# Performance work log

Hardware: AMD Instinct MI355X
Metric: run time of the kernel (lower is better)

## Reference

```python
import jax, jax.numpy as jnp
import numpy as np

B, T, C, H, E, MIN_E = 4, 2048, 1024, 128, 16, 2
IS_CAUSAL = False


def setup_inputs() -> dict:
    key = jax.random.key(0)
    ks = jax.random.split(key, 6)
    lim_qkv = float(np.sqrt(6.0 / (C + H)))
    inp = {
        "hidden_states": jax.random.normal(ks[0], (B, T, C), jnp.float32),
        "sim_matrix": jax.random.normal(ks[1], (C, E), jnp.float32),
        "gates": jnp.zeros((E,), jnp.float32),
        "q_proj": jax.random.uniform(ks[2], (E, C, H), jnp.float32, -lim_qkv, lim_qkv),
        "k_proj": jax.random.uniform(ks[3], (E, C, H), jnp.float32, -lim_qkv, lim_qkv),
        "v_proj": jax.random.uniform(ks[4], (E, C, H), jnp.float32, -lim_qkv, lim_qkv),
        "o_proj": jax.random.uniform(ks[5], (E, H, C), jnp.float32, -lim_qkv, lim_qkv),
    }
    return inp


def _forward(hidden_states, sim_matrix, gates, q_proj, k_proj, v_proj, o_proj):
    b, t, c = hidden_states.shape
    n = b * t
    x = hidden_states.reshape(n, c)

    # ---- gating (faithful to _gating_logic) ----
    xn = x / jnp.maximum(jnp.linalg.norm(x, axis=-1, keepdims=True), 1e-12)
    sn = sim_matrix / jnp.maximum(jnp.linalg.norm(sim_matrix, axis=0, keepdims=True), 1e-12)
    logits = xn @ sn - jax.nn.sigmoid(gates)          # [n, E]
    gated = jax.nn.relu(logits)
    # STE: forward = (gated > 0), backward = identity
    hard = (gated > 0).astype(gated.dtype)
    mask = gated + jax.lax.stop_gradient(hard - gated)
    inactive = (jnp.sum(hard, axis=1) == 0)
    # fallback: top-MIN_E logits for tokens with no active expert
    _, fb_idx = jax.lax.top_k(logits, MIN_E)
    fb = jnp.zeros((n, logits.shape[1]), gated.dtype).at[
        jnp.arange(n)[:, None], fb_idx].set(1.0)
    put = jax.lax.stop_gradient(inactive[:, None].astype(gated.dtype) * fb)
    mask = mask * (1.0 - put) + put                   # index_put semantics
    masked = jnp.where(mask > 0, gated, -jnp.inf)
    w = jax.nn.softmax(masked, axis=-1)               # routing weights [n, E]

    # ---- MoE dispatch/combine (dense-equivalent: w is exactly 0 where mask==0) ----
    def moe_proj(p):  # p: [E, C, H] -> [n, H]
        y = jnp.einsum('nc,ech->neh', x, p)
        return jnp.einsum('ne,neh->nh', w, y)

    q = moe_proj(q_proj).reshape(b, t, -1)
    k = moe_proj(k_proj).reshape(b, t, -1)
    v = moe_proj(v_proj).reshape(b, t, -1)

    # single-head SDPA, default scale 1/sqrt(head_dim)
    h = q.shape[-1]
    scores = jnp.einsum('bth,bsh->bts', q, k) / jnp.sqrt(jnp.asarray(h, q.dtype))
    if IS_CAUSAL and t > 1:
        causal = jnp.tril(jnp.ones((t, t), bool))
        scores = jnp.where(causal[None], scores, -jnp.inf)
    attn = jax.nn.softmax(scores, axis=-1)
    o = jnp.einsum('bts,bsh->bth', attn, v).reshape(n, h)

    # output MoE combine
    z = jnp.einsum('ne,nh->enh', w, o)                # [E, n, H]
    out = jnp.einsum('enh,ehc->nc', z, o_proj)
    return out.reshape(b, t, c)


def reference(hidden_states, sim_matrix, gates, q_proj, k_proj, v_proj, o_proj):
    return _forward(hidden_states, sim_matrix, gates, q_proj, k_proj, v_proj, o_proj)
```

## Files before the change

### kernel.cpp

```cpp
#include <hip/hip_runtime.h>
#include <hip/hip_bf16.h>
#include <math.h>

#define NBATCH 4
#define NT     2048
#define NC     1024
#define NH     128
#define NE     16
#define NTOK   (NBATCH * NT)
#define CAP    18432
#define NT2_MAX 152

typedef __bf16 bf16x8 __attribute__((ext_vector_type(8)));
typedef __bf16 bf16x4 __attribute__((ext_vector_type(4)));
typedef float  f32x4  __attribute__((ext_vector_type(4)));

__device__ __forceinline__ __bf16 f2bf(float f) { return (__bf16)f; }

#define BARRIER() __builtin_amdgcn_s_barrier()
#define SFENCE()  __builtin_amdgcn_sched_barrier(0)
#define VMWAIT(n) asm volatile("s_waitcnt vmcnt(" #n ")" ::: "memory")
#define LGKMWAIT0() asm volatile("s_waitcnt lgkmcnt(0)" ::: "memory")

__device__ __forceinline__ void gl_lds16(const void* g, void* l) {
  __builtin_amdgcn_global_load_lds((const __attribute__((address_space(1))) void*)g,
                                   (__attribute__((address_space(3))) void*)l, 16, 0, 0);
}

__device__ __forceinline__ const __bf16* swz_src(const __bf16* row0, size_t stride,
                                                 int tid, int i) {
  int lin = (tid + 256 * i) * 16;
  int r = lin >> 7, cb = lin & 127;
  return row0 + (size_t)r * stride + ((cb ^ ((r & 7) << 4)) >> 1);
}

__device__ __forceinline__ bool locate_tile(const int* __restrict__ counts, int ti,
                                            int& e_out, int& s0_out, int& seg_end_out) {
  int off = 0, nt = 0, e = -1, s0 = 0, seg_end = 0;
#pragma unroll
  for (int ee = 0; ee < NE; ee++) {
    int c = counts[ee];
    int tiles = (c + 127) >> 7;
    if (e < 0 && ti < nt + tiles) {
      e = ee;
      s0 = off + (ti - nt) * 128;
      seg_end = off + c;
    }
    nt += tiles;
    off += c;
  }
  if (e < 0 || s0 >= CAP) return false;
  if (seg_end > CAP) seg_end = CAP;
  e_out = e; s0_out = s0; seg_end_out = seg_end;
  return true;
}

__global__ void k_transpose_all(const float* __restrict__ qp, const float* __restrict__ kp,
                                const float* __restrict__ vp, const float* __restrict__ op,
                                __bf16* __restrict__ pqt, __bf16* __restrict__ pkt,
                                __bf16* __restrict__ pvt, __bf16* __restrict__ pot,
                                const float* __restrict__ sim, const float* __restrict__ gates,
                                double* __restrict__ snorm, double* __restrict__ sig,
                                int* __restrict__ ctrl) {
  __shared__ float tile[32][33];
  __shared__ double red[16][17];
  int z = blockIdx.y;
  int tid = threadIdx.x;
  if (z == 64) {
    if (blockIdx.x != 0) return;
    if (tid < 128) ctrl[tid] = 0;
    int e = tid & 15, chunk = tid >> 4;
    double a = 0.0;
#pragma unroll 4
    for (int j = 0; j < 64; j++) {
      double v = (double)sim[(chunk * 64 + j) * NE + e];
      a += v * v;
    }
    red[chunk][e] = a;
    __syncthreads();
    if (tid < 16) {
      double s = 0.0;
      for (int k = 0; k < 16; k++) s += red[k][tid];
      snorm[tid] = fmax(sqrt(s), 1e-12);
      sig[tid] = 1.0 / (1.0 + exp(-(double)gates[tid]));
    }
    return;
  }
  const float* in;
  __bf16* out;
  int R, Cd, g, r0, c0;
  if (z < 48) {
    int which = z >> 4; g = z & 15; R = 1024; Cd = 128;
    in = which == 0 ? qp : (which == 1 ? kp : vp);
    out = which == 0 ? pqt : (which == 1 ? pkt : pvt);
    r0 = (blockIdx.x >> 2) * 32; c0 = (blockIdx.x & 3) * 32;
  } else {
    g = z - 48; R = 128; Cd = 1024;
    in = op; out = pot;
    r0 = (blockIdx.x & 3) * 32; c0 = (blockIdx.x >> 2) * 32;
  }
  int tx = tid & 31, ty0 = tid >> 5;
  const float* src = in + (size_t)g * R * Cd;
  __bf16* dst = out + (size_t)g * R * Cd;
#pragma unroll
  for (int ty = ty0; ty < 32; ty += 8)
    tile[ty][tx] = src[(size_t)(r0 + ty) * Cd + (c0 + tx)];
  __syncthreads();
#pragma unroll
  for (int ty = ty0; ty < 32; ty += 8)
    dst[(size_t)(c0 + ty) * R + (r0 + tx)] = f2bf(tile[tx][ty]);
}

__global__ __launch_bounds__(256, 2) void k_gating3(const float* __restrict__ x,
                                                    const float* __restrict__ sim,
                                                    const double* __restrict__ snorm,
                                                    const double* __restrict__ sig,
                                                    float* __restrict__ w_all,
                                                    int* __restrict__ counts,
                                                    __bf16* __restrict__ xbf) {
  __shared__ union {
    struct {
      float xs_[16][66];
      float ss_[16][66];
    } s;
    double red[8][32][2][17];
  } u;
  __shared__ float w_lds[16][16];
  __shared__ int cnt_lds[16];
  int tid = threadIdx.x;
  if (tid < 16) cnt_lds[tid] = 0;
  int cg = tid & 31, tkg = tid >> 5;
  int tok0 = blockIdx.x * 16;

  double acc[2][17];
#pragma unroll
  for (int t = 0; t < 2; t++)
#pragma unroll
    for (int i = 0; i < 17; i++) acc[t][i] = 0.0;

  int xr0 = tid >> 4, xc4 = (tid & 15) * 4;
  int sr = tid >> 2, se4 = (tid & 3) * 4;

  float4 xa, sv;
  auto ldchunk = [&](int c0) {
    xa = *(const float4*)(x + (size_t)(tok0 + xr0) * NC + c0 + xc4);
    sv = *(const float4*)(sim + (size_t)(c0 + sr) * NE + se4);
  };
  auto stchunk = [&]() {
    *(float4*)&u.s.xs_[xr0][xc4] = xa;
    u.s.ss_[se4 + 0][sr] = sv.x;
    u.s.ss_[se4 + 1][sr] = sv.y;
    u.s.ss_[se4 + 2][sr] = sv.z;
    u.s.ss_[se4 + 3][sr] = sv.w;
  };
  auto stxbf = [&](int c0) {
    bf16x4 a;
    a[0]=f2bf(xa.x); a[1]=f2bf(xa.y); a[2]=f2bf(xa.z); a[3]=f2bf(xa.w);
    *(bf16x4*)(xbf + (size_t)(tok0 + xr0) * NC + c0 + xc4) = a;
  };

  ldchunk(0);
  for (int ch = 0; ch < 16; ch++) {
    stchunk();
    stxbf(ch * 64);
    __syncthreads();
    if (ch < 15) ldchunk((ch + 1) * 64);
    double xd[2][2];
#pragma unroll
    for (int t = 0; t < 2; t++) {
      float2 xv = *(const float2*)&u.s.xs_[tkg * 2 + t][cg * 2];
      xd[t][0] = (double)xv.x;
      xd[t][1] = (double)xv.y;
      acc[t][16] += xd[t][0] * xd[t][0] + xd[t][1] * xd[t][1];
    }
#pragma unroll
    for (int e = 0; e < 16; e++) {
      float2 sv2 = *(const float2*)&u.s.ss_[e][cg * 2];
      double s0 = (double)sv2.x, s1 = (double)sv2.y;
#pragma unroll
      for (int t = 0; t < 2; t++)
        acc[t][e] += xd[t][0] * s0 + xd[t][1] * s1;
    }
    __syncthreads();
  }

#pragma unroll
  for (int t = 0; t < 2; t++)
#pragma unroll
    for (int i = 0; i < 17; i++)
      u.red[tkg][cg][t][i] = acc[t][i];
  __syncthreads();

  if (tid < 16) {
    double dots[17];
    for (int i = 0; i < 17; i++) {
      double s = 0.0;
      for (int c = 0; c < 32; c++) s += u.red[tid >> 1][c][tid & 1][i];
      dots[i] = s;
    }
    double xn = fmax(sqrt(dots[16]), 1e-12);
    double logits[NE];
    unsigned act = 0;
    int cnt = 0;
    for (int ee = 0; ee < NE; ee++) {
      logits[ee] = dots[ee] / (xn * snorm[ee]) - sig[ee];
      if (logits[ee] > 0.0) { act |= 1u << ee; cnt++; }
    }
    if (cnt == 0) {
      int i1 = 0; double b1 = logits[0];
      for (int ee = 1; ee < NE; ee++) if (logits[ee] > b1) { b1 = logits[ee]; i1 = ee; }
      int i2 = -1; double b2 = -1e300;
      for (int ee = 0; ee < NE; ee++) if (ee != i1 && logits[ee] > b2) { b2 = logits[ee]; i2 = ee; }
      act = (1u << i1) | (1u << i2);
    }
    double m = -1e300;
    for (int ee = 0; ee < NE; ee++) if ((act >> ee) & 1) m = fmax(m, fmax(logits[ee], 0.0));
    double s = 0.0, wvv[NE];
    for (int ee = 0; ee < NE; ee++) {
      if ((act >> ee) & 1) { wvv[ee] = exp(fmax(logits[ee], 0.0) - m); s += wvv[ee]; }
      else wvv[ee] = 0.0;
    }
    for (int ee = 0; ee < NE; ee++) {
      if ((act >> ee) & 1) {
        w_lds[tid][ee] = (float)(wvv[ee] / s);
        atomicAdd(&cnt_lds[ee], 1);
      } else w_lds[tid][ee] = 0.0f;
    }
  }
  __syncthreads();
  w_all[(size_t)(tok0 + (tid >> 4)) * NE + (tid & 15)] = w_lds[tid >> 4][tid & 15];
  if (tid < 16 && cnt_lds[tid] > 0) atomicAdd(&counts[tid], cnt_lds[tid]);
}

__global__ void k_assign(const float* __restrict__ w_all, const int* __restrict__ counts,
                         int* __restrict__ cursors, int* __restrict__ slot_token,
                         float* __restrict__ slot_w, int* __restrict__ tok_slots,
                         int* __restrict__ tok_cnt) {
  int n = blockIdx.x * 256 + threadIdx.x;
  int lane = threadIdx.x & 63;
  int j = 0;
  int off = 0;
#pragma unroll
  for (int e = 0; e < NE; e++) {
    float w = w_all[(size_t)n * NE + e];
    bool a = w > 0.0f;
    unsigned long long mask = __ballot(a);
    if (mask) {
      int leader = (int)__ffsll((long long)mask) - 1;
      int base = 0;
      if (lane == leader) base = atomicAdd(&cursors[e], (int)__popcll(mask));
      base = __shfl(base, leader);
      if (a) {
        int pos = base + (int)__popcll(mask & ((1ULL << lane) - 1ULL));
        int s = off + pos;
        slot_token[s] = n;
        slot_w[s] = w;
        tok_slots[n * 16 + j] = s;
        j++;
      }
    }
    off += counts[e];
  }
  tok_cnt[n] = j;
}

__device__ __forceinline__ void mfma_block(const __bf16* As, const __bf16* Bs,
                                           int lane, int wrow, f32x4 acc[8]) {
  const char* Ab = (const char*)As;
  const char* Bb = (const char*)Bs;
  int arow = wrow + (lane & 15);
  int rb = lane & 15;
#pragma unroll
  for (int ks = 0; ks < 2; ks++) {
    int kb = ks * 64 + (lane >> 4) * 16;
    bf16x8 af = *(const bf16x8*)(Ab + arow * 128 + (kb ^ ((arow & 7) << 4)));
#pragma unroll
    for (int nt = 0; nt < 8; nt++) {
      int brow = nt * 16 + rb;
      bf16x8 bv = *(const bf16x8*)(Bb + brow * 128 + (kb ^ ((brow & 7) << 4)));
      acc[nt] = __builtin_amdgcn_mfma_f32_16x16x32_bf16(af, bv, acc[nt], 0, 0, 0);
    }
  }
}

__device__ __forceinline__ void mfma_block128(const __bf16* As, const __bf16* Bs,
                                              int lane, int wrow2, f32x4 acc[2][8]) {
  const char* Ab = (const char*)As;
  const char* Bb = (const char*)Bs;
  int rb = lane & 15;
#pragma unroll
  for (int ks = 0; ks < 2; ks++) {
    int kb = ks * 64 + (lane >> 4) * 16;
    int ar = wrow2 + rb;
    int sw = kb ^ ((ar & 7) << 4);
    bf16x8 af0 = *(const bf16x8*)(Ab + ar * 128 + sw);
    bf16x8 af1 = *(const bf16x8*)(Ab + (ar + 16) * 128 + sw);
#pragma unroll
    for (int nt = 0; nt < 8; nt++) {
      int brow = nt * 16 + rb;
      bf16x8 bv = *(const bf16x8*)(Bb + brow * 128 + (kb ^ ((brow & 7) << 4)));
      acc[0][nt] = __builtin_amdgcn_mfma_f32_16x16x32_bf16(af0, bv, acc[0][nt], 0, 0, 0);
      acc[1][nt] = __builtin_amdgcn_mfma_f32_16x16x32_bf16(af1, bv, acc[1][nt], 0, 0, 0);
    }
  }
}

__device__ __forceinline__ void mfma_regA(bf16x8 af0, bf16x8 af1, const __bf16* Bs,
                                          int lane, f32x4 acc[8]) {
  const char* Bb = (const char*)Bs;
  int rb = lane & 15;
#pragma unroll
  for (int ks = 0; ks < 2; ks++) {
    int kb = ks * 64 + (lane >> 4) * 16;
    bf16x8 af = ks ? af1 : af0;
#pragma unroll
    for (int nt = 0; nt < 8; nt++) {
      int brow = nt * 16 + rb;
      bf16x8 bv = *(const bf16x8*)(Bb + brow * 128 + (kb ^ ((brow & 7) << 4)));
      acc[nt] = __builtin_amdgcn_mfma_f32_16x16x32_bf16(af, bv, acc[nt], 0, 0, 0);
    }
  }
}

__global__ __launch_bounds__(256) void k_moe_qkv2(
    const __bf16* __restrict__ xbf, const int* __restrict__ slot_token,
    const __bf16* __restrict__ pq, const __bf16* __restrict__ pk, const __bf16* __restrict__ pv,
    const int* __restrict__ counts,
    __bf16* __restrict__ yq, __bf16* __restrict__ yk, __bf16* __restrict__ yv) {
  int id = blockIdx.x;
  int w = (id & 7) * (3 * NT2_MAX / 8) + (id >> 3);
  int ti = w / 3, p = w % 3;
  int e, s0, seg_end;
  if (!locate_tile(counts, ti, e, s0, seg_end)) return;
  const __bf16* Bt;
  __bf16* Yd;
  if (p == 0)      { Bt = pq; Yd = yq; }
  else if (p == 1) { Bt = pk; Yd = yk; }
  else             { Bt = pv; Yd = yv; }
  Bt += (size_t)e * NH * NC;

  __shared__ __bf16 As[2][128 * 64];
  __shared__ __bf16 Bs[2][128 * 64];
  int tid = threadIdx.x, lane = tid & 63, wid = tid >> 6, wrow2 = wid * 32;
  const __bf16* asrc[4];
  const __bf16* bsrc[4];
#pragma unroll
  for (int i = 0; i < 4; i++) {
    int lin = (tid + 256 * i) * 16;
    int r = lin >> 7, cb = lin & 127;
    int tok = slot_token[s0 + r] & (NTOK - 1);
    asrc[i] = xbf + (size_t)tok * NC + ((cb ^ ((r & 7) << 4)) >> 1);
  }
#pragma unroll
  for (int i = 0; i < 4; i++) bsrc[i] = swz_src(Bt, NC, tid, i);
  auto stage = [&](int buf, int k0) {
#pragma unroll
    for (int i = 0; i < 4; i++)
      gl_lds16(asrc[i] + k0, (char*)As[buf] + tid * 16 + i * 4096);
#pragma unroll
    for (int i = 0; i < 4; i++)
      gl_lds16(bsrc[i] + k0, (char*)Bs[buf] + tid * 16 + i * 4096);
  };

  f32x4 acc[2][8];
#pragma unroll
  for (int rf = 0; rf < 2; rf++)
#pragma unroll
    for (int i = 0; i < 8; i++) { f32x4 z = {0.f, 0.f, 0.f, 0.f}; acc[rf][i] = z; }

  stage(0, 0);
  stage(1, 64);
  VMWAIT(8); BARRIER(); SFENCE();
  int cur = 0;
  for (int t = 0; t <= 13; t++) {
    __builtin_amdgcn_s_setprio(1);
    mfma_block128(As[cur], Bs[cur], lane, wrow2, acc);
    __builtin_amdgcn_s_setprio(0);
    SFENCE();
    BARRIER();
    stage(cur, (t + 2) * 64);
    VMWAIT(8); BARRIER(); SFENCE();
    cur ^= 1;
  }
  __builtin_amdgcn_s_setprio(1);
  mfma_block128(As[cur], Bs[cur], lane, wrow2, acc);
  __builtin_amdgcn_s_setprio(0);
  SFENCE();
  VMWAIT(0); BARRIER(); SFENCE();
  __builtin_amdgcn_s_setprio(1);
  mfma_block128(As[cur ^ 1], Bs[cur ^ 1], lane, wrow2, acc);
  __builtin_amdgcn_s_setprio(0);

  int col = lane & 15, quad = lane >> 4;
#pragma unroll
  for (int rf = 0; rf < 2; rf++)
#pragma unroll
    for (int r = 0; r < 4; r++) {
      int s = s0 + wrow2 + rf * 16 + quad * 4 + r;
      if (s < seg_end) {
#pragma unroll
        for (int nt = 0; nt < 8; nt++)
          Yd[(size_t)s * NH + nt * 16 + col] = f2bf(acc[rf][nt][r]);
      }
    }
}

__global__ __launch_bounds__(256) void k_combine_qkv(
    const __bf16* __restrict__ yq, const __bf16* __restrict__ yk, const __bf16* __restrict__ yv,
    const int* __restrict__ tok_slots, const int* __restrict__ tok_cnt,
    const float* __restrict__ slot_w,
    __bf16* __restrict__ qb, __bf16* __restrict__ kb, __bf16* __restrict__ vt) {
  __shared__ __bf16 vtile[128][34];
  int tid = threadIdx.x;
  int tok0 = blockIdx.x * 32;
  int tt = tok0 + (tid >> 3);
  int h0 = (tid & 7) * 16;
  const __bf16* Y = blockIdx.y == 0 ? yq : (blockIdx.y == 1 ? yk : yv);
  int cnt = tok_cnt[tt];
  float acc[16];
#pragma unroll
  for (int i = 0; i < 16; i++) acc[i] = 0.f;
  for (int j = 0; j < cnt; j++) {
    int s = tok_slots[tt * 16 + j];
    if (s < CAP) {
      float w = slot_w[s];
      bf16x8 v0 = *(const bf16x8*)(Y + (size_t)s * NH + h0);
      bf16x8 v1 = *(const bf16x8*)(Y + (size_t)s * NH + h0 + 8);
#pragma unroll
      for (int i = 0; i < 8; i++) { acc[i] += w * (float)v0[i]; acc[8 + i] += w * (float)v1[i]; }
    }
  }
  if (blockIdx.y == 2) {
#pragma unroll
    for (int i = 0; i < 16; i++) vtile[h0 + i][tid >> 3] = f2bf(acc[i]);
    __syncthreads();
    int h = tid >> 1, tp = (tid & 1) * 16;
    int b = tok0 >> 11, trow = tok0 & 2047;
    __bf16* dst = vt + ((size_t)b * NH + h) * NT + trow + tp;
    bf16x8 o0, o1;
#pragma unroll
    for (int i = 0; i < 8; i++) { o0[i] = vtile[h][tp + i]; o1[i] = vtile[h][tp + 8 + i]; }
    *(bf16x8*)dst = o0;
    *(bf16x8*)(dst + 8) = o1;
  } else {
    float sc = blockIdx.y == 0 ? 0.12751744458115337f : 1.0f;
    __bf16* D = blockIdx.y == 0 ? qb : kb;
    bf16x8 o0, o1;
#pragma unroll
    for (int i = 0; i < 8; i++) { o0[i] = f2bf(acc[i] * sc); o1[i] = f2bf(acc[8 + i] * sc); }
    __bf16* d = D + (size_t)tt * NH + h0;
    *(bf16x8*)d = o0;
    *(bf16x8*)(d + 8) = o1;
  }
}

__global__ __launch_bounds__(256) void k_flash(const __bf16* __restrict__ q,
                                               const __bf16* __restrict__ k,
                                               const __bf16* __restrict__ vt,
                                               float* __restrict__ opart,
                                               float2* __restrict__ ml) {
  int id = blockIdx.x;
  int w = (id & 7) * 64 + (id >> 3);
  int b = w >> 7;
  int rem = w & 127;
  int spl = rem >> 5;
  int t0 = (rem & 31) * 64;
  const __bf16* qb = q + (size_t)b * NT * NH;
  const __bf16* kb = k + (size_t)b * NT * NH;
  const __bf16* vtb = vt + (size_t)b * NH * NT;

  __shared__ __bf16 Ks[2][128 * 64];
  __shared__ __bf16 Vs[2][128 * 64];
  __shared__ __bf16 Ps[2][64 * 64];
  int tid = threadIdx.x, lane = tid & 63, wid = tid >> 6, wrow = wid * 16;
  int colq = lane & 15, quad = lane >> 4;

  bf16x8 qf[4];
  {
    const __bf16* qr = qb + (size_t)(t0 + wrow + colq) * NH + quad * 8;
#pragma unroll
    for (int kk = 0; kk < 4; kk++) qf[kk] = *(const bf16x8*)(qr + kk * 32);
  }
  asm volatile("" :: "v"(qf[0]), "v"(qf[1]), "v"(qf[2]), "v"(qf[3]));
  SFENCE();

  auto stage_K = [&](int s0) {
#pragma unroll
    for (int c = 0; c < 2; c++)
#pragma unroll
      for (int i = 0; i < 4; i++)
        gl_lds16(swz_src(kb + (size_t)s0 * NH + c * 64, NH, tid, i),
                 (char*)Ks[c] + wid * 1024 + i * 4096);
  };
  auto stage_V = [&](int s0) {
#pragma unroll
    for (int c = 0; c < 2; c++)
#pragma unroll
      for (int i = 0; i < 4; i++)
        gl_lds16(swz_src(vtb + s0 + c * 64, NT, tid, i),
                 (char*)Vs[c] + wid * 1024 + i * 4096);
  };

  f32x4 oacc[8];
#pragma unroll
  for (int i = 0; i < 8; i++) { f32x4 z = {0.f, 0.f, 0.f, 0.f}; oacc[i] = z; }
  float mr[4], lr[4];
#pragma unroll
  for (int r = 0; r < 4; r++) { mr[r] = -1e30f; lr[r] = 0.f; }

  const int sbase = spl * 512;
  stage_K(sbase);
  stage_V(sbase);
  VMWAIT(8); BARRIER(); SFENCE();

  for (int t = 0; t < 4; t++) {
    f32x4 sacc[8];
#pragma unroll
    for (int i = 0; i < 8; i++) { f32x4 z = {0.f, 0.f, 0.f, 0.f}; sacc[i] = z; }
    __builtin_amdgcn_s_setprio(1);
    mfma_regA(qf[0], qf[1], Ks[0], lane, sacc);
    mfma_regA(qf[2], qf[3], Ks[1], lane, sacc);
    __builtin_amdgcn_s_setprio(0);
    SFENCE();
    BARRIER();
    if (t < 3) stage_K(sbase + (t + 1) * 128);

    float tm[4];
#pragma unroll
    for (int r = 0; r < 4; r++) {
      float v = sacc[0][r];
#pragma unroll
      for (int nt = 1; nt < 8; nt++) v = fmaxf(v, sacc[nt][r]);
      tm[r] = v;
    }
#pragma unroll
    for (int off = 1; off < 16; off <<= 1)
#pragma unroll
      for (int r = 0; r < 4; r++) tm[r] = fmaxf(tm[r], __shfl_xor(tm[r], off));
    float alpha[4], rs[4];
#pragma unroll
    for (int r = 0; r < 4; r++) {
      float mn = fmaxf(mr[r], tm[r]);
      alpha[r] = exp2f(mr[r] - mn);
      mr[r] = mn;
      rs[r] = 0.f;
    }
#pragma unroll
    for (int nt = 0; nt < 8; nt++) {
      char* pc = (char*)Ps[nt >> 2];
      int colb = ((nt & 3) * 16 + colq) * 2;
#pragma unroll
      for (int r = 0; r < 4; r++) {
        int row = wrow + quad * 4 + r;
        float p = exp2f(sacc[nt][r] - mr[r]);
        rs[r] += p;
        *(__bf16*)(pc + row * 128 + (colb ^ ((row & 7) << 4))) = f2bf(p);
      }
    }
#pragma unroll
    for (int off = 1; off < 16; off <<= 1)
#pragma unroll
      for (int r = 0; r < 4; r++) rs[r] += __shfl_xor(rs[r], off);
#pragma unroll
    for (int r = 0; r < 4; r++) lr[r] = alpha[r] * lr[r] + rs[r];
#pragma unroll
    for (int nt = 0; nt < 8; nt++)
#pragma unroll
      for (int r = 0; r < 4; r++) oacc[nt][r] *= alpha[r];

    LGKMWAIT0();
    if (t < 3) { VMWAIT(8); } else { VMWAIT(0); }
    BARRIER(); SFENCE();

    __builtin_amdgcn_s_setprio(1);
    mfma_block(Ps[0], Vs[0], lane, wrow, oacc);
    mfma_block(Ps[1], Vs[1], lane, wrow, oacc);
    __builtin_amdgcn_s_setprio(0);
    SFENCE();
    BARRIER();
    if (t < 3) {
      stage_V(sbase + (t + 1) * 128);
      VMWAIT(8); BARRIER(); SFENCE();
    }
  }

  size_t base = (size_t)(b * 4 + spl) * NT + t0;
#pragma unroll
  for (int r = 0; r < 4; r++) {
    size_t row = base + wrow + quad * 4 + r;
#pragma unroll
    for (int nt = 0; nt < 8; nt++)
      opart[row * NH + nt * 16 + colq] = oacc[nt][r];
  }
  if (colq == 0) {
#pragma unroll
    for (int r = 0; r < 4; r++) {
      float2 v; v.x = mr[r]; v.y = lr[r];
      ml[base + wrow + quad * 4 + r] = v;
    }
  }
}

__global__ __launch_bounds__(256) void k_gather_o(const float* __restrict__ opart,
                                                  const float2* __restrict__ ml,
                                                  const int* __restrict__ slot_token,
                                                  const int* __restrict__ counts,
                                                  __bf16* __restrict__ og) {
  int slot = blockIdx.x * 2 + (threadIdx.x >> 7);
  int h = threadIdx.x & 127;
  int total = 0;
#pragma unroll
  for (int e = 0; e < NE; e++) total += counts[e];
  if (total > CAP) total = CAP;
  if (slot >= total) return;
  int n = slot_token[slot];
  int b = n >> 11, trow = n & 2047;
  size_t rb = (size_t)b * 4 * NT + trow;
  float2 m0 = ml[rb], m1 = ml[rb + NT], m2 = ml[rb + 2 * NT], m3 = ml[rb + 3 * NT];
  float M = fmaxf(fmaxf(m0.x, m1.x), fmaxf(m2.x, m3.x));
  float e0 = exp2f(m0.x - M), e1 = exp2f(m1.x - M), e2 = exp2f(m2.x - M), e3 = exp2f(m3.x - M);
  float den = m0.y * e0 + m1.y * e1 + m2.y * e2 + m3.y * e3;
  float num = opart[rb * NH + h] * e0 + opart[(rb + NT) * NH + h] * e1 +
              opart[(rb + 2 * NT) * NH + h] * e2 + opart[(rb + 3 * NT) * NH + h] * e3;
  og[(size_t)slot * NH + h] = f2bf(num / den);
}

__global__ __launch_bounds__(256) void k_out2(
    const __bf16* __restrict__ og, const __bf16* __restrict__ pot,
    const int* __restrict__ counts, __bf16* __restrict__ zy) {
  int id = blockIdx.x;
  int w = (id & 7) * (4 * NT2_MAX / 8) + (id >> 3);
  int ti = w >> 2, p = w & 3;
  int e, s0, seg_end;
  if (!locate_tile(counts, ti, e, s0, seg_end)) return;
  int nc0 = p * 256;
  const __bf16* Bt = pot + (size_t)e * NC * NH;

  __shared__ __bf16 As[2][128 * 64];
  __shared__ __bf16 Bs[2][128 * 64];
  int tid = threadIdx.x, lane = tid & 63, wid = tid >> 6, wrow2 = wid * 32;
  const __bf16* asrc[4];
  const __bf16* bsrc[4];
#pragma unroll
  for (int i = 0; i < 4; i++) asrc[i] = swz_src(og + (size_t)s0 * NH, NH, tid, i);
#pragma unroll
  for (int i = 0; i < 4; i++) bsrc[i] = swz_src(Bt + (size_t)nc0 * NH, NH, tid, i);
  auto stageA = [&](int buf, int k0) {
#pragma unroll
    for (int i = 0; i < 4; i++)
      gl_lds16(asrc[i] + k0, (char*)As[buf] + tid * 16 + i * 4096);
  };
  auto stageB = [&](int buf, int k0, int noff) {
#pragma unroll
    for (int i = 0; i < 4; i++)
      gl_lds16(bsrc[i] + (size_t)noff * NH + k0, (char*)Bs[buf] + tid * 16 + i * 4096);
  };
  f32x4 acc[2][8];
  int col = lane & 15, quad = lane >> 4;
  auto store_acc = [&](int nco) {
#pragma unroll
    for (int rf = 0; rf < 2; rf++)
#pragma unroll
      for (int r = 0; r < 4; r++) {
        int s = s0 + wrow2 + rf * 16 + quad * 4 + r;
        if (s < seg_end) {
#pragma unroll
          for (int nt = 0; nt < 8; nt++)
            zy[(size_t)s * NC + nco + nt * 16 + col] = f2bf(acc[rf][nt][r]);
        }
      }
  };

#pragma unroll
  for (int rf = 0; rf < 2; rf++)
#pragma unroll
    for (int i = 0; i < 8; i++) { f32x4 z = {0.f, 0.f, 0.f, 0.f}; acc[rf][i] = z; }

  stageA(0, 0); stageB(0, 0, 0);
  stageA(1, 64); stageB(1, 64, 0);
  VMWAIT(8); BARRIER(); SFENCE();
  __builtin_amdgcn_s_setprio(1);
  mfma_block128(As[0], Bs[0], lane, wrow2, acc);
  __builtin_amdgcn_s_setprio(0);
  SFENCE();
  VMWAIT(0); BARRIER(); SFENCE();
  __builtin_amdgcn_s_setprio(1);
  mfma_block128(As[1], Bs[1], lane, wrow2, acc);
  __builtin_amdgcn_s_setprio(0);
  SFENCE();
  store_acc(nc0);
  BARRIER();
  stageB(0, 0, 128); stageB(1, 64, 128);
#pragma unroll
  for (int rf = 0; rf < 2; rf++)
#pragma unroll
    for (int i = 0; i < 8; i++) { f32x4 z = {0.f, 0.f, 0.f, 0.f}; acc[rf][i] = z; }
  VMWAIT(0); BARRIER(); SFENCE();
  __builtin_amdgcn_s_setprio(1);
  mfma_block128(As[0], Bs[0], lane, wrow2, acc);
  mfma_block128(As[1], Bs[1], lane, wrow2, acc);
  __builtin_amdgcn_s_setprio(0);
  store_acc(nc0 + 128);
}

__global__ __launch_bounds__(256) void k_combine_out(
    const __bf16* __restrict__ zy, const int* __restrict__ tok_slots,
    const int* __restrict__ tok_cnt, const float* __restrict__ slot_w,
    float* __restrict__ out) {
  int token = blockIdx.x;
  int c = threadIdx.x * 4;
  int cnt = tok_cnt[token];
  float a0 = 0.f, a1 = 0.f, a2 = 0.f, a3 = 0.f;
  for (int j = 0; j < cnt; j++) {
    int s = tok_slots[token * 16 + j];
    if (s < CAP) {
      float w = slot_w[s];
      bf16x4 z = *(const bf16x4*)&zy[(size_t)s * NC + c];
      a0 += w * (float)z[0];
      a1 += w * (float)z[1];
      a2 += w * (float)z[2];
      a3 += w * (float)z[3];
    }
  }
  float4 o = {a0, a1, a2, a3};
  *(float4*)&out[(size_t)token * NC + c] = o;
}

extern "C" void kernel_launch(void* const* d_in, const int* in_sizes, int n_in,
                              void* d_out, int out_size, void* d_ws, size_t ws_size,
                              hipStream_t stream) {
  const float* hs    = (const float*)d_in[0];
  const float* sim   = (const float*)d_in[1];
  const float* gates = (const float*)d_in[2];
  const float* qp    = (const float*)d_in[3];
  const float* kp    = (const float*)d_in[4];
  const float* vp    = (const float*)d_in[5];
  const float* op    = (const float*)d_in[6];
  float* out = (float*)d_out;
  char* ws = (char*)d_ws;

  const size_t M = 1048576;
  __bf16* PQT = (__bf16*)(ws + 0 * M);
  __bf16* PKT = (__bf16*)(ws + 4 * M);
  __bf16* PVT = (__bf16*)(ws + 8 * M);
  __bf16* POT = (__bf16*)(ws + 12 * M);
  __bf16* Qb  = (__bf16*)(ws + 16 * M);
  __bf16* Kb  = (__bf16*)(ws + 18 * M);
  __bf16* VT  = (__bf16*)(ws + 22 * M);
  float*  WALL = (float*)(ws + 28 * M);
  int*    STOK = (int*)(ws + 28 * M + 524288);
  float*  SW   = (float*)(ws + 28 * M + 1048576);
  int*    TSL  = (int*)(ws + 28 * M + 1572864);
  int*    TCN  = (int*)(ws + 28 * M + 2097152);
  double* SNORM = (double*)(ws + 28 * M + 2129920);
  double* SIG   = SNORM + 16;
  int* CNT = (int*)(ws + 28 * M + 2130432);
  int* CUR = CNT + 40;
  __bf16* XBF = (__bf16*)(ws + 32 * M);
  __bf16* YQ = (__bf16*)(ws + 72 * M);
  __bf16* YK = (__bf16*)(ws + 77 * M);
  __bf16* YV = (__bf16*)(ws + 82 * M);
  float*  OP2 = (float*)(ws + 32 * M);
  float2* MLB = (float2*)(ws + 50 * M);
  __bf16* OG = (__bf16*)(ws + 52 * M);
  __bf16* ZY = (__bf16*)(ws + 60 * M);

  k_transpose_all<<<dim3(128, 65), 256, 0, stream>>>(qp, kp, vp, op, PQT, PKT, PVT, POT,
                                                     sim, gates, SNORM, SIG, CNT);
  k_gating3<<<NTOK / 16, 256, 0, stream>>>(hs, sim, SNORM, SIG, WALL, CNT, XBF);
  k_assign<<<NTOK / 256, 256, 0, stream>>>(WALL, CNT, CUR, STOK, SW, TSL, TCN);
  k_moe_qkv2<<<3 * NT2_MAX, 256, 0, stream>>>(XBF, STOK, PQT, PKT, PVT, CNT, YQ, YK, YV);
  k_combine_qkv<<<dim3(NTOK / 32, 3), 256, 0, stream>>>(YQ, YK, YV, TSL, TCN, SW, Qb, Kb, VT);
  k_flash<<<512, 256, 0, stream>>>(Qb, Kb, VT, OP2, MLB);
  k_gather_o<<<CAP / 2, 256, 0, stream>>>(OP2, MLB, STOK, CNT, OG);
  k_out2<<<4 * NT2_MAX, 256, 0, stream>>>(OG, POT, CNT, ZY);
  k_combine_out<<<NTOK, 256, 0, stream>>>(ZY, TSL, TCN, SW, out);
}
```

Baseline: 265.8 us.

## Fold sim-norm/sigmoid into gating, merge weight transpose into assign kernel

```diff
diff --git a/kernel.cpp b/kernel.cpp
--- a/kernel.cpp
+++ b/kernel.cpp
@@ -55,66 +55,9 @@
   return true;
 }
 
-__global__ void k_transpose_all(const float* __restrict__ qp, const float* __restrict__ kp,
-                                const float* __restrict__ vp, const float* __restrict__ op,
-                                __bf16* __restrict__ pqt, __bf16* __restrict__ pkt,
-                                __bf16* __restrict__ pvt, __bf16* __restrict__ pot,
-                                const float* __restrict__ sim, const float* __restrict__ gates,
-                                double* __restrict__ snorm, double* __restrict__ sig,
-                                int* __restrict__ ctrl) {
-  __shared__ float tile[32][33];
-  __shared__ double red[16][17];
-  int z = blockIdx.y;
-  int tid = threadIdx.x;
-  if (z == 64) {
-    if (blockIdx.x != 0) return;
-    if (tid < 128) ctrl[tid] = 0;
-    int e = tid & 15, chunk = tid >> 4;
-    double a = 0.0;
-#pragma unroll 4
-    for (int j = 0; j < 64; j++) {
-      double v = (double)sim[(chunk * 64 + j) * NE + e];
-      a += v * v;
-    }
-    red[chunk][e] = a;
-    __syncthreads();
-    if (tid < 16) {
-      double s = 0.0;
-      for (int k = 0; k < 16; k++) s += red[k][tid];
-      snorm[tid] = fmax(sqrt(s), 1e-12);
-      sig[tid] = 1.0 / (1.0 + exp(-(double)gates[tid]));
-    }
-    return;
-  }
-  const float* in;
-  __bf16* out;
-  int R, Cd, g, r0, c0;
-  if (z < 48) {
-    int which = z >> 4; g = z & 15; R = 1024; Cd = 128;
-    in = which == 0 ? qp : (which == 1 ? kp : vp);
-    out = which == 0 ? pqt : (which == 1 ? pkt : pvt);
-    r0 = (blockIdx.x >> 2) * 32; c0 = (blockIdx.x & 3) * 32;
-  } else {
-    g = z - 48; R = 128; Cd = 1024;
-    in = op; out = pot;
-    r0 = (blockIdx.x & 3) * 32; c0 = (blockIdx.x >> 2) * 32;
-  }
-  int tx = tid & 31, ty0 = tid >> 5;
-  const float* src = in + (size_t)g * R * Cd;
-  __bf16* dst = out + (size_t)g * R * Cd;
-#pragma unroll
-  for (int ty = ty0; ty < 32; ty += 8)
-    tile[ty][tx] = src[(size_t)(r0 + ty) * Cd + (c0 + tx)];
-  __syncthreads();
-#pragma unroll
-  for (int ty = ty0; ty < 32; ty += 8)
-    dst[(size_t)(c0 + ty) * R + (r0 + tx)] = f2bf(tile[tx][ty]);
-}
-
 __global__ __launch_bounds__(256, 2) void k_gating3(const float* __restrict__ x,
                                                     const float* __restrict__ sim,
-                                                    const double* __restrict__ snorm,
-                                                    const double* __restrict__ sig,
+                                                    const float* __restrict__ gates,
                                                     float* __restrict__ w_all,
                                                     int* __restrict__ counts,
                                                     __bf16* __restrict__ xbf) {
@@ -125,10 +68,16 @@
     } s;
     double red[8][32][2][17];
   } u;
+  __shared__ double snred[32][17];
+  __shared__ double snorm_lds[16];
+  __shared__ double sig_lds[16];
   __shared__ float w_lds[16][16];
   __shared__ int cnt_lds[16];
   int tid = threadIdx.x;
-  if (tid < 16) cnt_lds[tid] = 0;
+  if (tid < 16) {
+    cnt_lds[tid] = 0;
+    sig_lds[tid] = 1.0 / (1.0 + exp(-(double)gates[tid]));
+  }
   int cg = tid & 31, tkg = tid >> 5;
   int tok0 = blockIdx.x * 16;
 
@@ -137,6 +86,10 @@
   for (int t = 0; t < 2; t++)
 #pragma unroll
     for (int i = 0; i < 17; i++) acc[t][i] = 0.0;
+  double sn[16];
+#pragma unroll
+  for (int i = 0; i < 16; i++) sn[i] = 0.0;
+  bool dosn = tid < 64;
 
   int xr0 = tid >> 4, xc4 = (tid & 15) * 4;
   int sr = tid >> 2, se4 = (tid & 3) * 4;
@@ -180,6 +133,7 @@
 #pragma unroll
       for (int t = 0; t < 2; t++)
         acc[t][e] += xd[t][0] * s0 + xd[t][1] * s1;
+      if (dosn) sn[e] += s0 * s0 + s1 * s1;
     }
     __syncthreads();
   }
@@ -189,6 +143,16 @@
 #pragma unroll
     for (int i = 0; i < 17; i++)
       u.red[tkg][cg][t][i] = acc[t][i];
+  if (tid < 32)
+#pragma unroll
+    for (int e = 0; e < 16; e++) snred[tid][e] = sn[e];
+  __syncthreads();
+
+  if (tid < 16) {
+    double s = 0.0;
+    for (int c = 0; c < 32; c++) s += snred[c][tid];
+    snorm_lds[tid] = fmax(sqrt(s), 1e-12);
+  }
   __syncthreads();
 
   if (tid < 16) {
@@ -203,7 +167,7 @@
     unsigned act = 0;
     int cnt = 0;
     for (int ee = 0; ee < NE; ee++) {
-      logits[ee] = dots[ee] / (xn * snorm[ee]) - sig[ee];
+      logits[ee] = dots[ee] / (xn * snorm_lds[ee]) - sig_lds[ee];
       if (logits[ee] > 0.0) { act |= 1u << ee; cnt++; }
     }
     if (cnt == 0) {
@@ -232,36 +196,73 @@
   if (tid < 16 && cnt_lds[tid] > 0) atomicAdd(&counts[tid], cnt_lds[tid]);
 }
 
-__global__ void k_assign(const float* __restrict__ w_all, const int* __restrict__ counts,
-                         int* __restrict__ cursors, int* __restrict__ slot_token,
-                         float* __restrict__ slot_w, int* __restrict__ tok_slots,
-                         int* __restrict__ tok_cnt) {
-  int n = blockIdx.x * 256 + threadIdx.x;
-  int lane = threadIdx.x & 63;
-  int j = 0;
-  int off = 0;
-#pragma unroll
-  for (int e = 0; e < NE; e++) {
-    float w = w_all[(size_t)n * NE + e];
-    bool a = w > 0.0f;
-    unsigned long long mask = __ballot(a);
-    if (mask) {
-      int leader = (int)__ffsll((long long)mask) - 1;
-      int base = 0;
-      if (lane == leader) base = atomicAdd(&cursors[e], (int)__popcll(mask));
-      base = __shfl(base, leader);
-      if (a) {
-        int pos = base + (int)__popcll(mask & ((1ULL << lane) - 1ULL));
-        int s = off + pos;
-        slot_token[s] = n;
-        slot_w[s] = w;
-        tok_slots[n * 16 + j] = s;
-        j++;
+__global__ __launch_bounds__(256) void k_assign_tr(
+    const float* __restrict__ w_all, const int* __restrict__ counts,
+    int* __restrict__ cursors, int* __restrict__ slot_token,
+    float* __restrict__ slot_w, int* __restrict__ tok_slots, int* __restrict__ tok_cnt,
+    const float* __restrict__ qp, const float* __restrict__ kp,
+    const float* __restrict__ vp, const float* __restrict__ op,
+    __bf16* __restrict__ pqt, __bf16* __restrict__ pkt,
+    __bf16* __restrict__ pvt, __bf16* __restrict__ pot) {
+  __shared__ float tile[32][33];
+  int id = blockIdx.x;
+  int tid = threadIdx.x;
+
+  if (id < 32) {
+    int n = id * 256 + tid;
+    int lane = tid & 63;
+    int j = 0;
+    int off = 0;
+#pragma unroll
+    for (int e = 0; e < NE; e++) {
+      float w = w_all[(size_t)n * NE + e];
+      bool a = w > 0.0f;
+      unsigned long long mask = __ballot(a);
+      if (mask) {
+        int leader = (int)__ffsll((long long)mask) - 1;
+        int base = 0;
+        if (lane == leader) base = atomicAdd(&cursors[e], (int)__popcll(mask));
+        base = __shfl(base, leader);
+        if (a) {
+          int pos = base + (int)__popcll(mask & ((1ULL << lane) - 1ULL));
+          int s = off + pos;
+          slot_token[s] = n;
+          slot_w[s] = w;
+          tok_slots[n * 16 + j] = s;
+          j++;
+        }
       }
-    }
-    off += counts[e];
-  }
-  tok_cnt[n] = j;
+      off += counts[e];
+    }
+    tok_cnt[n] = j;
+    return;
+  }
+
+  int t2 = id - 32;
+  int z = t2 >> 7, xb = t2 & 127;
+  const float* in;
+  __bf16* out;
+  int R, Cd, g, r0, c0;
+  if (z < 48) {
+    int which = z >> 4; g = z & 15; R = 1024; Cd = 128;
+    in = which == 0 ? qp : (which == 1 ? kp : vp);
+    out = which == 0 ? pqt : (which == 1 ? pkt : pvt);
+    r0 = (xb >> 2) * 32; c0 = (xb & 3) * 32;
+  } else {
+    g = z - 48; R = 128; Cd = 1024;
+    in = op; out = pot;
+    r0 = (xb & 3) * 32; c0 = (xb >> 2) * 32;
+  }
+  int tx = tid & 31, ty0 = tid >> 5;
+  const float* src = in + (size_t)g * R * Cd;
+  __bf16* dst = out + (size_t)g * R * Cd;
+#pragma unroll
+  for (int ty = ty0; ty < 32; ty += 8)
+    tile[ty][tx] = src[(size_t)(r0 + ty) * Cd + (c0 + tx)];
+  __syncthreads();
+#pragma unroll
+  for (int ty = ty0; ty < 32; ty += 8)
+    dst[(size_t)(c0 + ty) * R + (r0 + tx)] = f2bf(tile[tx][ty]);
 }
 
 __device__ __forceinline__ void mfma_block(const __bf16* As, const __bf16* Bs,
@@ -752,8 +753,6 @@
   float*  SW   = (float*)(ws + 28 * M + 1048576);
   int*    TSL  = (int*)(ws + 28 * M + 1572864);
   int*    TCN  = (int*)(ws + 28 * M + 2097152);
-  double* SNORM = (double*)(ws + 28 * M + 2129920);
-  double* SIG   = SNORM + 16;
   int* CNT = (int*)(ws + 28 * M + 2130432);
   int* CUR = CNT + 40;
   __bf16* XBF = (__bf16*)(ws + 32 * M);
@@ -765,10 +764,11 @@
   __bf16* OG = (__bf16*)(ws + 52 * M);
   __bf16* ZY = (__bf16*)(ws + 60 * M);
 
-  k_transpose_all<<<dim3(128, 65), 256, 0, stream>>>(qp, kp, vp, op, PQT, PKT, PVT, POT,
-                                                     sim, gates, SNORM, SIG, CNT);
-  k_gating3<<<NTOK / 16, 256, 0, stream>>>(hs, sim, SNORM, SIG, WALL, CNT, XBF);
-  k_assign<<<NTOK / 256, 256, 0, stream>>>(WALL, CNT, CUR, STOK, SW, TSL, TCN);
+  hipMemsetAsync(CNT, 0, 512, stream);
+
+  k_gating3<<<NTOK / 16, 256, 0, stream>>>(hs, sim, gates, WALL, CNT, XBF);
+  k_assign_tr<<<32 + 64 * 128, 256, 0, stream>>>(WALL, CNT, CUR, STOK, SW, TSL, TCN,
+                                                 qp, kp, vp, op, PQT, PKT, PVT, POT);
   k_moe_qkv2<<<3 * NT2_MAX, 256, 0, stream>>>(XBF, STOK, PQT, PKT, PVT, CNT, YQ, YK, YV);
   k_combine_qkv<<<dim3(NTOK / 32, 3), 256, 0, stream>>>(YQ, YK, YV, TSL, TCN, SW, Qb, Kb, VT);
   k_flash<<<512, 256, 0, stream>>>(Qb, Kb, VT, OP2, MLB);
```

Measured after the change: 251.7 us. 1.06x faster.
